# Optimization experiments

Hardware: AMD Instinct MI355X
Metric: run time of the kernel (lower is better)

Reference implementation:

```python
import jax, jax.numpy as jnp
import numpy as np

N_NODES = 100000
N_EDGES = 1600000
NODE_DIM = 3
EDGE_DIM = 32
HIDDEN = 128
OUT_DIM = 3
N_GRAPHS = 64


def _lin(key, fan_in, fan_out):
    k1, k2 = jax.random.split(key)
    s = 1.0 / np.sqrt(fan_in)
    W = jax.random.uniform(k1, (fan_in, fan_out), minval=-s, maxval=s, dtype=jnp.float32)
    b = jax.random.uniform(k2, (fan_out,), minval=-s, maxval=s, dtype=jnp.float32)
    return W, b


def setup_inputs() -> dict:
    key = jax.random.key(0)
    ks = jax.random.split(key, 16)
    x = jax.random.normal(ks[0], (N_NODES, NODE_DIM), dtype=jnp.float32)
    edge_index = jax.random.randint(ks[1], (2, N_EDGES), 0, N_NODES, dtype=jnp.int32)
    edge_attr = jax.random.normal(ks[2], (N_EDGES, EDGE_DIM), dtype=jnp.float32)
    batch = jnp.sort(jax.random.randint(ks[3], (N_NODES,), 0, N_GRAPHS, dtype=jnp.int32))
    # conv1: CGConv at channels=NODE_DIM, in = 2*NODE_DIM + EDGE_DIM
    Wf1, bf1 = _lin(ks[4], 2 * NODE_DIM + EDGE_DIM, NODE_DIM)
    Ws1, bs1 = _lin(ks[5], 2 * NODE_DIM + EDGE_DIM, NODE_DIM)
    Wp, bp = _lin(ks[6], NODE_DIM, HIDDEN)
    # two hidden CGConvs at channels=HIDDEN
    Wf2, bf2 = _lin(ks[7], 2 * HIDDEN + EDGE_DIM, HIDDEN)
    Ws2, bs2 = _lin(ks[8], 2 * HIDDEN + EDGE_DIM, HIDDEN)
    Wf3, bf3 = _lin(ks[9], 2 * HIDDEN + EDGE_DIM, HIDDEN)
    Ws3, bs3 = _lin(ks[10], 2 * HIDDEN + EDGE_DIM, HIDDEN)
    W1, b1 = _lin(ks[11], HIDDEN, HIDDEN)
    W2, b2 = _lin(ks[12], HIDDEN, OUT_DIM)
    return dict(x=x, edge_index=edge_index, edge_attr=edge_attr, batch=batch,
                Wf1=Wf1, bf1=bf1, Ws1=Ws1, bs1=bs1, Wp=Wp, bp=bp,
                Wf2=Wf2, bf2=bf2, Ws2=Ws2, bs2=bs2,
                Wf3=Wf3, bf3=bf3, Ws3=Ws3, bs3=bs3,
                W1=W1, b1=b1, W2=W2, b2=b2)


def _cgconv(x, src, dst, edge_attr, Wf, bf, Ws, bs):
    # z = [x_i (target), x_j (source), e_ij]; message = sigmoid(lin_f(z)) * softplus(lin_s(z))
    z = jnp.concatenate([x[dst], x[src], edge_attr], axis=-1)  # [E, 2C+F]
    m = jax.nn.sigmoid(z @ Wf + bf) * jax.nn.softplus(z @ Ws + bs)  # [E, C]
    agg = jax.ops.segment_sum(m, dst, num_segments=x.shape[0])
    return x + agg


def reference(x, edge_index, edge_attr, batch,
              Wf1, bf1, Ws1, bs1, Wp, bp,
              Wf2, bf2, Ws2, bs2, Wf3, bf3, Ws3, bs3,
              W1, b1, W2, b2):
    src, dst = edge_index[0], edge_index[1]
    h = _cgconv(x, src, dst, edge_attr, Wf1, bf1, Ws1, bs1)
    h = jax.nn.relu(h @ Wp + bp)
    h = jax.nn.relu(_cgconv(h, src, dst, edge_attr, Wf2, bf2, Ws2, bs2))
    h = jax.nn.relu(_cgconv(h, src, dst, edge_attr, Wf3, bf3, Ws3, bs3))
    # global mean pool over graphs
    sums = jax.ops.segment_sum(h, batch, num_segments=N_GRAPHS)
    counts = jax.ops.segment_sum(jnp.ones((h.shape[0],), h.dtype), batch, num_segments=N_GRAPHS)
    pooled = sums / jnp.maximum(counts, 1.0)[:, None]
    g = jax.nn.relu(pooled @ W1 + b1)
    return g @ W2 + b2
```

## Files before the change

kernel.cpp:

```cpp
#include <hip/hip_runtime.h>
#include <hip/hip_bf16.h>


#define N_NODES 100000
#define N_EDGES 1600000
#define HID 128
#define SCAN_BLOCKS 391

typedef unsigned int uint;
typedef short bf16x8 __attribute__((ext_vector_type(8)));
typedef float f32x4 __attribute__((ext_vector_type(4)));

__device__ inline float bflo(uint u) { return __uint_as_float(u << 16); }
__device__ inline float bfhi(uint u) { return __uint_as_float(u & 0xffff0000u); }
__device__ inline uint pack_bf16_2(float a, float b) {
  uint ua = __float_as_uint(a), ub = __float_as_uint(b);
  ua = (ua + 0x7fffu + ((ua >> 16) & 1u)) >> 16;
  ub = (ub + 0x7fffu + ((ub >> 16) & 1u)) >> 16;
  return ua | (ub << 16);
}
__device__ inline float sigmoidf_(float x) {
  return __builtin_amdgcn_rcpf(1.f + __expf(-x));
}
__device__ inline float softplusf_(float x) {
  return fmaxf(x, 0.f) + __logf(1.f + __expf(-fabsf(x)));
}

__global__ __launch_bounds__(256) void hist_k(const int* __restrict__ ei,
                                              int* __restrict__ deg) {
  int e = blockIdx.x * 256 + threadIdx.x;
  if (e >= N_EDGES) return;
  atomicAdd(&deg[ei[N_EDGES + e]], 1);
}

__global__ __launch_bounds__(256) void scan1_k(const int* __restrict__ deg,
                                               int* __restrict__ rowptr,
                                               int* __restrict__ bsums) {
  __shared__ int s[256];
  int i = blockIdx.x * 256 + threadIdx.x;
  int v = (i < N_NODES) ? deg[i] : 0;
  s[threadIdx.x] = v;
  __syncthreads();
  for (int off = 1; off < 256; off <<= 1) {
    int t = (threadIdx.x >= off) ? s[threadIdx.x - off] : 0;
    __syncthreads();
    s[threadIdx.x] += t;
    __syncthreads();
  }
  if (i < N_NODES) rowptr[i] = s[threadIdx.x] - v;
  if (threadIdx.x == 255) bsums[blockIdx.x] = s[255];
}

__global__ __launch_bounds__(512) void scan2_k(int* __restrict__ bsums) {
  __shared__ int s[512];
  int t = threadIdx.x;
  int v = (t < SCAN_BLOCKS) ? bsums[t] : 0;
  s[t] = v;
  __syncthreads();
  for (int off = 1; off < 512; off <<= 1) {
    int x = (t >= off) ? s[t - off] : 0;
    __syncthreads();
    s[t] += x;
    __syncthreads();
  }
  if (t < SCAN_BLOCKS) bsums[t] = s[t] - v;
}

__global__ __launch_bounds__(256) void scan3_k(int* __restrict__ rowptr,
                                               const int* __restrict__ bsums,
                                               int* __restrict__ cur) {
  int i = blockIdx.x * 256 + threadIdx.x;
  if (i < N_NODES) {
    int r = rowptr[i] + bsums[blockIdx.x];
    rowptr[i] = r;
    cur[i] = r;
  }
  if (i == 0) rowptr[N_NODES] = N_EDGES;
}

__global__ __launch_bounds__(256) void scatter_k(const int* __restrict__ ei,
                                                 int* __restrict__ cur,
                                                 uint4* __restrict__ csr) {
  int e = blockIdx.x * 256 + threadIdx.x;
  if (e >= N_EDGES) return;
  int d = ei[N_EDGES + e];
  int pos = atomicAdd(&cur[d], 1);
  csr[pos] = make_uint4((uint)ei[e], (uint)e, (uint)d, 0u);
}

__global__ __launch_bounds__(256) void ea_pack(const float* __restrict__ ea,
                                               const uint4* __restrict__ csr,
                                               uint4* __restrict__ eab) {
  long long t = (long long)blockIdx.x * 256 + threadIdx.x;
  int p = (int)(t >> 2), q = (int)(t & 3);
  if (p >= N_EDGES) return;
  uint e = csr[p].y;
  const float4* er = (const float4*)(ea + (long long)e * 32 + q * 8);
  float4 a0 = er[0], a1 = er[1];
  uint4 pk;
  pk.x = pack_bf16_2(a0.x, a0.y);
  pk.y = pack_bf16_2(a0.z, a0.w);
  pk.z = pack_bf16_2(a1.x, a1.y);
  pk.w = pack_bf16_2(a1.z, a1.w);
  eab[(long long)p * 4 + q] = pk;
}

__global__ __launch_bounds__(256) void conv1_edge(
    const float* __restrict__ x, const int* __restrict__ ei,
    const float* __restrict__ ea,
    const float* __restrict__ Wf, const float* __restrict__ bf,
    const float* __restrict__ Ws, const float* __restrict__ bs,
    float* __restrict__ agg1) {
  int e = blockIdx.x * 256 + threadIdx.x;
  if (e >= N_EDGES) return;
  int src = ei[e], dst = ei[N_EDGES + e];
  float z[38];
#pragma unroll
  for (int k = 0; k < 3; ++k) z[k] = x[dst * 3 + k];
#pragma unroll
  for (int k = 0; k < 3; ++k) z[3 + k] = x[src * 3 + k];
  const float4* er4 = (const float4*)(ea + (long long)e * 32);
#pragma unroll
  for (int k = 0; k < 8; ++k) {
    float4 v = er4[k];
    z[6 + 4 * k + 0] = v.x;
    z[6 + 4 * k + 1] = v.y;
    z[6 + 4 * k + 2] = v.z;
    z[6 + 4 * k + 3] = v.w;
  }
#pragma unroll
  for (int c = 0; c < 3; ++c) {
    float f = bf[c], s = bs[c];
#pragma unroll
    for (int k = 0; k < 38; ++k) {
      f = fmaf(z[k], Wf[k * 3 + c], f);
      s = fmaf(z[k], Ws[k * 3 + c], s);
    }
    atomicAdd(&agg1[dst * 3 + c], sigmoidf_(f) * softplusf_(s));
  }
}

__global__ __launch_bounds__(256) void proj_kernel(
    const float* __restrict__ x, const float* __restrict__ agg1,
    const float* __restrict__ Wp, const float* __restrict__ bp,
    float* __restrict__ h) {
  long long i = (long long)blockIdx.x * 256 + threadIdx.x;
  if (i >= (long long)N_NODES * HID) return;
  int n = (int)(i >> 7), j = (int)(i & 127);
  float v0 = x[n * 3 + 0] + agg1[n * 3 + 0];
  float v1 = x[n * 3 + 1] + agg1[n * 3 + 1];
  float v2 = x[n * 3 + 2] + agg1[n * 3 + 2];
  float acc = bp[j];
  acc = fmaf(v0, Wp[0 * HID + j], acc);
  acc = fmaf(v1, Wp[1 * HID + j], acc);
  acc = fmaf(v2, Wp[2 * HID + j], acc);
  h[i] = fmaxf(acc, 0.f);
}

#define BM 64
#define BK 32

__global__ __launch_bounds__(256) void node_gemm2(
    const float* __restrict__ h, const float* __restrict__ Wf,
    const float* __restrict__ Ws, const float* __restrict__ bf,
    const float* __restrict__ bs, uint* __restrict__ Pb) {
  __shared__ float As[BK][BM + 4];
  __shared__ float BfS[BK][BM + 4];
  __shared__ float BsS[BK][BM + 4];
  int jblk = blockIdx.x;
  int part = jblk >> 1;
  int colbase = (jblk & 1) * 64;
  int rowoff = part * 128;
  int m0 = blockIdx.y * BM;
  int tid = threadIdx.x, tx = tid & 15, ty = tid >> 4;
  float accF[4][4] = {}, accS[4][4] = {};
  for (int k0 = 0; k0 < 128; k0 += BK) {
#pragma unroll
    for (int i = 0; i < 2; ++i) {
      int f = tid + i * 256;
      int r = f >> 3, c4 = (f & 7) * 4;
      float4 v = {0.f, 0.f, 0.f, 0.f};
      int row = m0 + r;
      if (row < N_NODES)
        v = *(const float4*)&h[(long long)row * 128 + k0 + c4];
      As[c4 + 0][r] = v.x; As[c4 + 1][r] = v.y;
      As[c4 + 2][r] = v.z; As[c4 + 3][r] = v.w;
    }
#pragma unroll
    for (int i = 0; i < 2; ++i) {
      int f = tid + i * 256;
      int r = f >> 4, c4 = (f & 15) * 4;
      *(float4*)&BfS[r][c4] =
          *(const float4*)&Wf[(long long)(k0 + r + rowoff) * 128 + colbase + c4];
      *(float4*)&BsS[r][c4] =
          *(const float4*)&Ws[(long long)(k0 + r + rowoff) * 128 + colbase + c4];
    }
    __syncthreads();
#pragma unroll
    for (int k = 0; k < BK; ++k) {
      float4 a = *(const float4*)&As[k][ty * 4];
      float4 bF = *(const float4*)&BfS[k][tx * 4];
      float4 bS = *(const float4*)&BsS[k][tx * 4];
      float av[4] = {a.x, a.y, a.z, a.w};
      float bFv[4] = {bF.x, bF.y, bF.z, bF.w};
      float bSv[4] = {bS.x, bS.y, bS.z, bS.w};
#pragma unroll
      for (int i = 0; i < 4; ++i)
#pragma unroll
        for (int j = 0; j < 4; ++j) {
          accF[i][j] = fmaf(av[i], bFv[j], accF[i][j]);
          accS[i][j] = fmaf(av[i], bSv[j], accS[i][j]);
        }
    }
    __syncthreads();
  }
  float fbias[4] = {0.f, 0.f, 0.f, 0.f}, sbias[4] = {0.f, 0.f, 0.f, 0.f};
  if (part == 0) {
#pragma unroll
    for (int j = 0; j < 4; ++j) {
      fbias[j] = bf[colbase + tx * 4 + j];
      sbias[j] = bs[colbase + tx * 4 + j];
    }
  }
#pragma unroll
  for (int i = 0; i < 4; ++i) {
    int row = m0 + ty * 4 + i;
    if (row < N_NODES) {
      uint4 o;
      o.x = pack_bf16_2(accF[i][0] + fbias[0], accS[i][0] + sbias[0]);
      o.y = pack_bf16_2(accF[i][1] + fbias[1], accS[i][1] + sbias[1]);
      o.z = pack_bf16_2(accF[i][2] + fbias[2], accS[i][2] + sbias[2]);
      o.w = pack_bf16_2(accF[i][3] + fbias[3], accS[i][3] + sbias[3]);
      *(uint4*)&Pb[(long long)row * 256 + part * 128 + colbase + tx * 4] = o;
    }
  }
}

__global__ __launch_bounds__(256) void w_prep(const float* __restrict__ Wf,
                                              const float* __restrict__ Ws,
                                              uint* __restrict__ Btg) {
  int t = threadIdx.x;
  const float* W = (t < 128) ? Wf : Ws;
  int c = t & 127;
#pragma unroll
  for (int kk = 0; kk < 16; ++kk) {
    float a = W[(256 + 2 * kk) * 128 + c];
    float b = W[(256 + 2 * kk + 1) * 128 + c];
    Btg[t * 16 + kk] = pack_bf16_2(a, b);
  }
}

#define EMSG_EB 64
#define LSTR 20
#define CAP 16
__global__ __launch_bounds__(256, 4) void edge_msg(
    const uint* __restrict__ Pb, const uint4* __restrict__ eab,
    const uint* __restrict__ Btg, const uint4* __restrict__ csr,
    const int* __restrict__ rowptr, float* __restrict__ h) {
  __shared__ uint Alds[EMSG_EB * LSTR];
  __shared__ uint Blds[256 * LSTR];
  __shared__ float accL[CAP * 128];
  __shared__ int dstL[64], srcL[64], liL[64];
  __shared__ int dlist[CAP], compL[CAP];
  __shared__ int nDistS;
  int tid = threadIdx.x;
  int j0 = blockIdx.x * EMSG_EB;
  {
    int r = tid >> 2, q = tid & 3;
    uint4 v = eab[(long long)j0 * 4 + tid];
    *(uint4*)&Alds[r * LSTR + q * 4] = v;
  }
  {
    const uint4* s4 = (const uint4*)(Btg + tid * 16);
    uint4 v0 = s4[0], v1 = s4[1], v2 = s4[2], v3 = s4[3];
    uint* d = &Blds[tid * LSTR];
    *(uint4*)(d + 0) = v0; *(uint4*)(d + 4) = v1;
    *(uint4*)(d + 8) = v2; *(uint4*)(d + 12) = v3;
  }
#pragma unroll
  for (int i = 0; i < (CAP * 128) / 256; ++i) accL[tid + i * 256] = 0.f;
  if (tid < 64) {
    uint4 cj = csr[j0 + tid];
    int d = (int)cj.z;
    dstL[tid] = d;
    srcL[tid] = (int)cj.x;
    int dprev = __shfl_up(d, 1, 64);
    bool flag = (tid == 0) || (d != dprev);
    unsigned long long m = __ballot(flag);
    unsigned long long pre = (tid == 63) ? ~0ull : ((1ull << (tid + 1)) - 1);
    int li = __popcll(m & pre) - 1;
    liL[tid] = li;
    if (flag && li < CAP) {
      dlist[li] = d;
      int r0 = rowptr[d], r1 = rowptr[d + 1];
      compL[li] = ((r0 == j0 + tid) && (r1 <= j0 + EMSG_EB)) ? 1 : 0;
    }
    if (tid == 0) nDistS = __popcll(m);
  }
  __syncthreads();
  int wave = tid >> 6, lane = tid & 63;
  int c0w = wave * 32;
  int l15 = lane & 15, lq = lane >> 4;
  bf16x8 afr[4], bfr[4];
#pragma unroll
  for (int mt = 0; mt < 4; ++mt)
    afr[mt] = *(const bf16x8*)&Alds[(mt * 16 + l15) * LSTR + lq * 4];
  int chs0 = c0w + l15, chs1 = c0w + 16 + l15;
  bfr[0] = *(const bf16x8*)&Blds[chs0 * LSTR + lq * 4];
  bfr[1] = *(const bf16x8*)&Blds[chs1 * LSTR + lq * 4];
  bfr[2] = *(const bf16x8*)&Blds[(128 + chs0) * LSTR + lq * 4];
  bfr[3] = *(const bf16x8*)&Blds[(128 + chs1) * LSTR + lq * 4];
  f32x4 acc[4][4];
#pragma unroll
  for (int mt = 0; mt < 4; ++mt)
#pragma unroll
    for (int nt = 0; nt < 4; ++nt) {
      f32x4 z = {0.f, 0.f, 0.f, 0.f};
      acc[mt][nt] = __builtin_amdgcn_mfma_f32_16x16x32_bf16(afr[mt], bfr[nt], z, 0, 0, 0);
    }
#pragma unroll
  for (int mt = 0; mt < 4; ++mt) {
    int o = mt * 16 + lq * 4;
    int dsts[4], lis[4];
#pragma unroll
    for (int reg = 0; reg < 4; ++reg) {
      dsts[reg] = dstL[o + reg];
      lis[reg] = liL[o + reg];
    }
#pragma unroll
    for (int cp = 0; cp < 2; ++cp) {
      int c = (cp ? chs1 : chs0);
      float mr[4];
#pragma unroll
      for (int reg = 0; reg < 4; ++reg) {
        uint gd = Pb[(long long)dsts[reg] * 256 + c];
        uint gs = Pb[(long long)srcL[o + reg] * 256 + 128 + c];
        float f = acc[mt][cp][reg] + bflo(gd) + bflo(gs);
        float s = acc[mt][2 + cp][reg] + bfhi(gd) + bfhi(gs);
        mr[reg] = sigmoidf_(f) * softplusf_(s);
      }
      float racc = mr[0];
      int cl = lis[0], cd = dsts[0];
#pragma unroll
      for (int reg = 1; reg < 4; ++reg) {
        if (lis[reg] == cl) {
          racc += mr[reg];
        } else {
          if (cl < CAP) atomicAdd(&accL[cl * 128 + c], racc);
          else atomicAdd(&h[(long long)cd * HID + c], racc);
          cl = lis[reg]; cd = dsts[reg]; racc = mr[reg];
        }
      }
      if (cl < CAP) atomicAdd(&accL[cl * 128 + c], racc);
      else atomicAdd(&h[(long long)cd * HID + c], racc);
    }
  }
  __syncthreads();
  int nD = nDistS;
  if (nD > CAP) nD = CAP;
  int c = tid & 127;
  for (int li = tid >> 7; li < nD; li += 2) {
    int d = dlist[li];
    float v = accL[li * 128 + c];
    float* hp = &h[(long long)d * HID + c];
    if (compL[li]) {
      *hp = fmaxf(*hp + v, 0.f);
    } else {
      atomicAdd(hp, v);
    }
  }
}

__global__ __launch_bounds__(256) void relu_k(float* __restrict__ h) {
  const int total = N_NODES * HID / 4;
  for (int i = blockIdx.x * 256 + threadIdx.x; i < total; i += gridDim.x * 256) {
    float4 v = ((float4*)h)[i];
    v.x = fmaxf(v.x, 0.f); v.y = fmaxf(v.y, 0.f);
    v.z = fmaxf(v.z, 0.f); v.w = fmaxf(v.w, 0.f);
    ((float4*)h)[i] = v;
  }
}

#define POOL_NODES 128
__global__ __launch_bounds__(128) void pool2(
    const float* __restrict__ h, const int* __restrict__ batch,
    float* __restrict__ sums, float* __restrict__ cnts) {
  int n0 = blockIdx.x * POOL_NODES;
  if (n0 >= N_NODES) return;
  int t = threadIdx.x;
  int nEnd = n0 + POOL_NODES;
  if (nEnd > N_NODES) nEnd = N_NODES;
  float acc = 0.f;
  int bcur = batch[n0];
  int cnt = 0;
  for (int n = n0; n < nEnd; ++n) {
    int b = batch[n];
    if (b != bcur) {
      atomicAdd(&sums[bcur * HID + t], acc);
      if (t == 0) atomicAdd(&cnts[bcur], (float)cnt);
      acc = 0.f; cnt = 0; bcur = b;
    }
    acc += h[(long long)n * HID + t];
    ++cnt;
  }
  atomicAdd(&sums[bcur * HID + t], acc);
  if (t == 0) atomicAdd(&cnts[bcur], (float)cnt);
}

__global__ __launch_bounds__(128) void mlpA(
    const float* __restrict__ sums, const float* __restrict__ cnts,
    const float* __restrict__ W1, const float* __restrict__ b1,
    float* __restrict__ g) {
  __shared__ float pl[HID];
  int gr = blockIdx.x, j = threadIdx.x;
  float cnt = fmaxf(cnts[gr], 1.f);
  pl[j] = sums[gr * HID + j] / cnt;
  __syncthreads();
  float acc = b1[j];
#pragma unroll 8
  for (int k = 0; k < HID; ++k) acc = fmaf(pl[k], W1[k * HID + j], acc);
  g[gr * HID + j] = fmaxf(acc, 0.f);
}

__global__ __launch_bounds__(256) void mlpB(
    const float* __restrict__ g, const float* __restrict__ W2,
    const float* __restrict__ b2, float* __restrict__ out) {
  int t = threadIdx.x;
  if (t >= 64 * 3) return;
  int gr = t / 3, o = t % 3;
  float acc = b2[o];
#pragma unroll 8
  for (int k = 0; k < HID; ++k) acc = fmaf(g[gr * HID + k], W2[k * 3 + o], acc);
  out[t] = acc;
}

extern "C" void kernel_launch(void* const* d_in, const int* in_sizes, int n_in,
                              void* d_out, int out_size, void* d_ws, size_t ws_size,
                              hipStream_t stream) {
  const float* x   = (const float*)d_in[0];
  const int*   ei  = (const int*)d_in[1];
  const float* ea  = (const float*)d_in[2];
  const int*   bat = (const int*)d_in[3];
  const float* Wf1 = (const float*)d_in[4];
  const float* bf1 = (const float*)d_in[5];
  const float* Ws1 = (const float*)d_in[6];
  const float* bs1 = (const float*)d_in[7];
  const float* Wp  = (const float*)d_in[8];
  const float* bp  = (const float*)d_in[9];
  const float* Wf2 = (const float*)d_in[10];
  const float* bf2 = (const float*)d_in[11];
  const float* Ws2 = (const float*)d_in[12];
  const float* bs2 = (const float*)d_in[13];
  const float* Wf3 = (const float*)d_in[14];
  const float* bf3 = (const float*)d_in[15];
  const float* Ws3 = (const float*)d_in[16];
  const float* bs3 = (const float*)d_in[17];
  const float* W1  = (const float*)d_in[18];
  const float* b1  = (const float*)d_in[19];
  const float* W2  = (const float*)d_in[20];
  const float* b2  = (const float*)d_in[21];
  float* out = (float*)d_out;

  char* w = (char*)d_ws;
  size_t off = 0;
  auto alloc = [&](size_t bytes) {
    void* p = w + off;
    off += (bytes + 255) & ~(size_t)255;
    return p;
  };
  int*   deg    = (int*)alloc((size_t)N_NODES * 4);
  int*   rowptr = (int*)alloc((size_t)(N_NODES + 1) * 4);
  int*   cur    = (int*)alloc((size_t)N_NODES * 4);
  int*   bsums  = (int*)alloc((size_t)512 * 4);
  uint4* csr    = (uint4*)alloc((size_t)N_EDGES * 16);
  float* agg1   = (float*)alloc((size_t)N_NODES * 3 * 4);
  float* h      = (float*)alloc((size_t)N_NODES * HID * 4);
  uint*  Pb     = (uint*)alloc((size_t)N_NODES * 256 * 4);
  uint4* eab    = (uint4*)alloc((size_t)N_EDGES * 64);
  float* sums   = (float*)alloc((size_t)64 * HID * 4);
  float* cnts   = (float*)alloc((size_t)64 * 4);
  float* g      = (float*)alloc((size_t)64 * HID * 4);
  uint*  Btg    = (uint*)alloc((size_t)256 * 16 * 4);
  (void)ws_size;

  hipMemsetAsync(deg, 0, (size_t)N_NODES * 4, stream);
  hist_k<<<(N_EDGES + 255) / 256, 256, 0, stream>>>(ei, deg);
  scan1_k<<<SCAN_BLOCKS, 256, 0, stream>>>(deg, rowptr, bsums);
  scan2_k<<<1, 512, 0, stream>>>(bsums);
  scan3_k<<<SCAN_BLOCKS, 256, 0, stream>>>(rowptr, bsums, cur);
  scatter_k<<<(N_EDGES + 255) / 256, 256, 0, stream>>>(ei, cur, csr);
  ea_pack<<<(N_EDGES * 4 + 255) / 256, 256, 0, stream>>>(ea, csr, eab);

  hipMemsetAsync(agg1, 0, (size_t)N_NODES * 3 * 4, stream);
  conv1_edge<<<(N_EDGES + 255) / 256, 256, 0, stream>>>(x, ei, ea, Wf1, bf1, Ws1, bs1, agg1);
  proj_kernel<<<(N_NODES * HID + 255) / 256, 256, 0, stream>>>(x, agg1, Wp, bp, h);

  dim3 ngrid2(4, (N_NODES + BM - 1) / BM);
  int eblocks = N_EDGES / EMSG_EB;

  node_gemm2<<<ngrid2, 256, 0, stream>>>(h, Wf2, Ws2, bf2, bs2, Pb);
  w_prep<<<1, 256, 0, stream>>>(Wf2, Ws2, Btg);
  edge_msg<<<eblocks, 256, 0, stream>>>(Pb, eab, Btg, csr, rowptr, h);
  relu_k<<<4096, 256, 0, stream>>>(h);

  node_gemm2<<<ngrid2, 256, 0, stream>>>(h, Wf3, Ws3, bf3, bs3, Pb);
  w_prep<<<1, 256, 0, stream>>>(Wf3, Ws3, Btg);
  edge_msg<<<eblocks, 256, 0, stream>>>(Pb, eab, Btg, csr, rowptr, h);
  relu_k<<<4096, 256, 0, stream>>>(h);

  hipMemsetAsync(sums, 0, (size_t)(64 * HID + 64) * 4, stream);
  pool2<<<(N_NODES + POOL_NODES - 1) / POOL_NODES, POOL_NODES, 0, stream>>>(h, bat, sums, cnts);
  mlpA<<<64, 128, 0, stream>>>(sums, cnts, W1, b1, g);
  mlpB<<<1, 256, 0, stream>>>(g, W2, b2, out);
}
```

Measured before the change: 2.038 ms.

## Switch node GEMM to bf16 MFMA with bf16 activation copy; simplify edge atomics

Replaces the fp32 SIMT node GEMM with an MFMA bf16 kernel that reads a packed bf16 copy of h, produced by the projection and ReLU kernels, plus pre-packed weights. This removes the fp32 FMA-bound GEMM and halves its input bandwidth. In exchange it adds the bf16 copy writes and a weight-prep launch, and lowers GEMM input precision. The edge message kernel also drops its run-length merging of same-destination values and issues one atomic per edge value.

```diff
diff --git a/kernel.cpp b/kernel.cpp
--- a/kernel.cpp
+++ b/kernel.cpp
@@ -140,98 +140,105 @@
   }
 }
 
-__global__ __launch_bounds__(256) void proj_kernel(
+__global__ __launch_bounds__(256) void proj2(
     const float* __restrict__ x, const float* __restrict__ agg1,
     const float* __restrict__ Wp, const float* __restrict__ bp,
-    float* __restrict__ h) {
+    float* __restrict__ h, uint* __restrict__ hb) {
   long long i = (long long)blockIdx.x * 256 + threadIdx.x;
-  if (i >= (long long)N_NODES * HID) return;
-  int n = (int)(i >> 7), j = (int)(i & 127);
+  if (i >= (long long)N_NODES * 64) return;
+  int n = (int)(i >> 6), jp = (int)(i & 63);
+  int j0 = jp * 2;
   float v0 = x[n * 3 + 0] + agg1[n * 3 + 0];
   float v1 = x[n * 3 + 1] + agg1[n * 3 + 1];
   float v2 = x[n * 3 + 2] + agg1[n * 3 + 2];
-  float acc = bp[j];
-  acc = fmaf(v0, Wp[0 * HID + j], acc);
-  acc = fmaf(v1, Wp[1 * HID + j], acc);
-  acc = fmaf(v2, Wp[2 * HID + j], acc);
-  h[i] = fmaxf(acc, 0.f);
-}
-
-#define BM 64
-#define BK 32
-
-__global__ __launch_bounds__(256) void node_gemm2(
-    const float* __restrict__ h, const float* __restrict__ Wf,
-    const float* __restrict__ Ws, const float* __restrict__ bf,
-    const float* __restrict__ bs, uint* __restrict__ Pb) {
-  __shared__ float As[BK][BM + 4];
-  __shared__ float BfS[BK][BM + 4];
-  __shared__ float BsS[BK][BM + 4];
-  int jblk = blockIdx.x;
-  int part = jblk >> 1;
-  int colbase = (jblk & 1) * 64;
-  int rowoff = part * 128;
-  int m0 = blockIdx.y * BM;
-  int tid = threadIdx.x, tx = tid & 15, ty = tid >> 4;
-  float accF[4][4] = {}, accS[4][4] = {};
-  for (int k0 = 0; k0 < 128; k0 += BK) {
-#pragma unroll
-    for (int i = 0; i < 2; ++i) {
-      int f = tid + i * 256;
-      int r = f >> 3, c4 = (f & 7) * 4;
-      float4 v = {0.f, 0.f, 0.f, 0.f};
-      int row = m0 + r;
-      if (row < N_NODES)
-        v = *(const float4*)&h[(long long)row * 128 + k0 + c4];
-      As[c4 + 0][r] = v.x; As[c4 + 1][r] = v.y;
-      As[c4 + 2][r] = v.z; As[c4 + 3][r] = v.w;
-    }
-#pragma unroll
-    for (int i = 0; i < 2; ++i) {
-      int f = tid + i * 256;
-      int r = f >> 4, c4 = (f & 15) * 4;
-      *(float4*)&BfS[r][c4] =
-          *(const float4*)&Wf[(long long)(k0 + r + rowoff) * 128 + colbase + c4];
-      *(float4*)&BsS[r][c4] =
-          *(const float4*)&Ws[(long long)(k0 + r + rowoff) * 128 + colbase + c4];
-    }
-    __syncthreads();
-#pragma unroll
-    for (int k = 0; k < BK; ++k) {
-      float4 a = *(const float4*)&As[k][ty * 4];
-      float4 bF = *(const float4*)&BfS[k][tx * 4];
-      float4 bS = *(const float4*)&BsS[k][tx * 4];
-      float av[4] = {a.x, a.y, a.z, a.w};
-      float bFv[4] = {bF.x, bF.y, bF.z, bF.w};
-      float bSv[4] = {bS.x, bS.y, bS.z, bS.w};
-#pragma unroll
-      for (int i = 0; i < 4; ++i)
-#pragma unroll
-        for (int j = 0; j < 4; ++j) {
-          accF[i][j] = fmaf(av[i], bFv[j], accF[i][j]);
-          accS[i][j] = fmaf(av[i], bSv[j], accS[i][j]);
-        }
-    }
-    __syncthreads();
-  }
-  float fbias[4] = {0.f, 0.f, 0.f, 0.f}, sbias[4] = {0.f, 0.f, 0.f, 0.f};
-  if (part == 0) {
-#pragma unroll
-    for (int j = 0; j < 4; ++j) {
-      fbias[j] = bf[colbase + tx * 4 + j];
-      sbias[j] = bs[colbase + tx * 4 + j];
-    }
-  }
-#pragma unroll
-  for (int i = 0; i < 4; ++i) {
-    int row = m0 + ty * 4 + i;
+  float a0 = bp[j0], a1 = bp[j0 + 1];
+  a0 = fmaf(v0, Wp[0 * HID + j0], a0);
+  a0 = fmaf(v1, Wp[1 * HID + j0], a0);
+  a0 = fmaf(v2, Wp[2 * HID + j0], a0);
+  a1 = fmaf(v0, Wp[0 * HID + j0 + 1], a1);
+  a1 = fmaf(v1, Wp[1 * HID + j0 + 1], a1);
+  a1 = fmaf(v2, Wp[2 * HID + j0 + 1], a1);
+  a0 = fmaxf(a0, 0.f);
+  a1 = fmaxf(a1, 0.f);
+  *(float2*)&h[(long long)n * HID + j0] = make_float2(a0, a1);
+  hb[(long long)n * 64 + jp] = pack_bf16_2(a0, a1);
+}
+
+__global__ __launch_bounds__(256) void w_prep2(const float* __restrict__ Wf,
+                                               const float* __restrict__ Ws,
+                                               uint* __restrict__ Wpk) {
+  int row = blockIdx.x * 256 + threadIdx.x;
+  int pm = row >> 7;
+  int c = row & 127;
+  const float* W = (pm & 1) ? Ws : Wf;
+  int rowoff = (pm >> 1) * 128;
+  for (int kk = 0; kk < 64; ++kk) {
+    float a = W[(rowoff + 2 * kk) * 128 + c];
+    float b = W[(rowoff + 2 * kk + 1) * 128 + c];
+    Wpk[row * 64 + kk] = pack_bf16_2(a, b);
+  }
+}
+
+#define NG_STR 68
+__global__ __launch_bounds__(256, 4) void node_gemmM(
+    const uint* __restrict__ hb, const uint* __restrict__ Wpk,
+    const float* __restrict__ bf, const float* __restrict__ bs,
+    uint* __restrict__ Pb) {
+  __shared__ uint Alds[64 * NG_STR];
+  int part = blockIdx.x;
+  int m0 = blockIdx.y * 64;
+  int tid = threadIdx.x;
+  {
+    int r = tid >> 2, q = tid & 3;
+    int row = m0 + r;
+    uint* d = &Alds[r * NG_STR + q * 16];
     if (row < N_NODES) {
-      uint4 o;
-      o.x = pack_bf16_2(accF[i][0] + fbias[0], accS[i][0] + sbias[0]);
-      o.y = pack_bf16_2(accF[i][1] + fbias[1], accS[i][1] + sbias[1]);
-      o.z = pack_bf16_2(accF[i][2] + fbias[2], accS[i][2] + sbias[2]);
-      o.w = pack_bf16_2(accF[i][3] + fbias[3], accS[i][3] + sbias[3]);
-      *(uint4*)&Pb[(long long)row * 256 + part * 128 + colbase + tx * 4] = o;
+      const uint4* s4 = (const uint4*)&hb[(long long)row * 64 + q * 16];
+      uint4 v0 = s4[0], v1 = s4[1], v2 = s4[2], v3 = s4[3];
+      *(uint4*)(d + 0) = v0; *(uint4*)(d + 4) = v1;
+      *(uint4*)(d + 8) = v2; *(uint4*)(d + 12) = v3;
+    } else {
+      uint4 z = make_uint4(0, 0, 0, 0);
+      *(uint4*)(d + 0) = z; *(uint4*)(d + 4) = z;
+      *(uint4*)(d + 8) = z; *(uint4*)(d + 12) = z;
+    }
+  }
+  __syncthreads();
+  int wave = tid >> 6, lane = tid & 63;
+  int l15 = lane & 15, lq = lane >> 4;
+  int arow = wave * 16 + l15;
+  const uint* WpF = Wpk + (part * 2 + 0) * 128 * 64;
+  const uint* WpS = Wpk + (part * 2 + 1) * 128 * 64;
+  f32x4 accF[8], accS[8];
+#pragma unroll
+  for (int nt = 0; nt < 8; ++nt) {
+    f32x4 z = {0.f, 0.f, 0.f, 0.f};
+    accF[nt] = z;
+    accS[nt] = z;
+  }
+#pragma unroll
+  for (int ks = 0; ks < 4; ++ks) {
+    bf16x8 afr = *(const bf16x8*)&Alds[arow * NG_STR + ks * 16 + lq * 4];
+#pragma unroll
+    for (int nt = 0; nt < 8; ++nt) {
+      bf16x8 bF = *(const bf16x8*)&WpF[(nt * 16 + l15) * 64 + ks * 16 + lq * 4];
+      bf16x8 bS = *(const bf16x8*)&WpS[(nt * 16 + l15) * 64 + ks * 16 + lq * 4];
+      accF[nt] = __builtin_amdgcn_mfma_f32_16x16x32_bf16(afr, bF, accF[nt], 0, 0, 0);
+      accS[nt] = __builtin_amdgcn_mfma_f32_16x16x32_bf16(afr, bS, accS[nt], 0, 0, 0);
+    }
+  }
+#pragma unroll
+  for (int nt = 0; nt < 8; ++nt) {
+    int c = nt * 16 + l15;
+    float fb = (part == 0) ? bf[c] : 0.f;
+    float sb = (part == 0) ? bs[c] : 0.f;
+#pragma unroll
+    for (int reg = 0; reg < 4; ++reg) {
+      int node = m0 + wave * 16 + lq * 4 + reg;
+      if (node < N_NODES) {
+        Pb[(long long)node * 256 + part * 128 + c] =
+            pack_bf16_2(accF[nt][reg] + fb, accS[nt][reg] + sb);
+      }
     }
   }
 }
@@ -321,38 +328,29 @@
 #pragma unroll
   for (int mt = 0; mt < 4; ++mt) {
     int o = mt * 16 + lq * 4;
-    int dsts[4], lis[4];
+    int dsts[4], srcs[4], lis[4];
 #pragma unroll
     for (int reg = 0; reg < 4; ++reg) {
       dsts[reg] = dstL[o + reg];
+      srcs[reg] = srcL[o + reg];
       lis[reg] = liL[o + reg];
     }
 #pragma unroll
     for (int cp = 0; cp < 2; ++cp) {
       int c = (cp ? chs1 : chs0);
-      float mr[4];
 #pragma unroll
       for (int reg = 0; reg < 4; ++reg) {
         uint gd = Pb[(long long)dsts[reg] * 256 + c];
-        uint gs = Pb[(long long)srcL[o + reg] * 256 + 128 + c];
+        uint gs = Pb[(long long)srcs[reg] * 256 + 128 + c];
         float f = acc[mt][cp][reg] + bflo(gd) + bflo(gs);
         float s = acc[mt][2 + cp][reg] + bfhi(gd) + bfhi(gs);
-        mr[reg] = sigmoidf_(f) * softplusf_(s);
-      }
-      float racc = mr[0];
-      int cl = lis[0], cd = dsts[0];
-#pragma unroll
-      for (int reg = 1; reg < 4; ++reg) {
-        if (lis[reg] == cl) {
-          racc += mr[reg];
+        float mr = sigmoidf_(f) * softplusf_(s);
+        if (lis[reg] < CAP) {
+          atomicAdd(&accL[lis[reg] * 128 + c], mr);
         } else {
-          if (cl < CAP) atomicAdd(&accL[cl * 128 + c], racc);
-          else atomicAdd(&h[(long long)cd * HID + c], racc);
-          cl = lis[reg]; cd = dsts[reg]; racc = mr[reg];
+          atomicAdd(&h[(long long)dsts[reg] * HID + c], mr);
         }
       }
-      if (cl < CAP) atomicAdd(&accL[cl * 128 + c], racc);
-      else atomicAdd(&h[(long long)cd * HID + c], racc);
     }
   }
   __syncthreads();
@@ -368,6 +366,21 @@
     } else {
       atomicAdd(hp, v);
     }
+  }
+}
+
+__global__ __launch_bounds__(256) void relu2(float* __restrict__ h,
+                                             uint* __restrict__ hb) {
+  const int total = N_NODES * 32;
+  for (int i = blockIdx.x * 256 + threadIdx.x; i < total; i += gridDim.x * 256) {
+    float4 v = ((float4*)h)[i];
+    v.x = fmaxf(v.x, 0.f); v.y = fmaxf(v.y, 0.f);
+    v.z = fmaxf(v.z, 0.f); v.w = fmaxf(v.w, 0.f);
+    ((float4*)h)[i] = v;
+    uint2 o;
+    o.x = pack_bf16_2(v.x, v.y);
+    o.y = pack_bf16_2(v.z, v.w);
+    *(uint2*)&hb[(long long)i * 2] = o;
   }
 }
 
@@ -475,12 +488,14 @@
   uint4* csr    = (uint4*)alloc((size_t)N_EDGES * 16);
   float* agg1   = (float*)alloc((size_t)N_NODES * 3 * 4);
   float* h      = (float*)alloc((size_t)N_NODES * HID * 4);
+  uint*  hb     = (uint*)alloc((size_t)N_NODES * 64 * 4);
   uint*  Pb     = (uint*)alloc((size_t)N_NODES * 256 * 4);
   uint4* eab    = (uint4*)alloc((size_t)N_EDGES * 64);
   float* sums   = (float*)alloc((size_t)64 * HID * 4);
   float* cnts   = (float*)alloc((size_t)64 * 4);
   float* g      = (float*)alloc((size_t)64 * HID * 4);
   uint*  Btg    = (uint*)alloc((size_t)256 * 16 * 4);
+  uint*  Wpk    = (uint*)alloc((size_t)512 * 64 * 4);
   (void)ws_size;
 
   hipMemsetAsync(deg, 0, (size_t)N_NODES * 4, stream);
@@ -493,17 +508,19 @@
 
   hipMemsetAsync(agg1, 0, (size_t)N_NODES * 3 * 4, stream);
   conv1_edge<<<(N_EDGES + 255) / 256, 256, 0, stream>>>(x, ei, ea, Wf1, bf1, Ws1, bs1, agg1);
-  proj_kernel<<<(N_NODES * HID + 255) / 256, 256, 0, stream>>>(x, agg1, Wp, bp, h);
-
-  dim3 ngrid2(4, (N_NODES + BM - 1) / BM);
+  proj2<<<(N_NODES * 64 + 255) / 256, 256, 0, stream>>>(x, agg1, Wp, bp, h, hb);
+
+  dim3 nggrid(2, (N_NODES + 63) / 64);
   int eblocks = N_EDGES / EMSG_EB;
 
-  node_gemm2<<<ngrid2, 256, 0, stream>>>(h, Wf2, Ws2, bf2, bs2, Pb);
+  w_prep2<<<2, 256, 0, stream>>>(Wf2, Ws2, Wpk);
+  node_gemmM<<<nggrid, 256, 0, stream>>>(hb, Wpk, bf2, bs2, Pb);
   w_prep<<<1, 256, 0, stream>>>(Wf2, Ws2, Btg);
   edge_msg<<<eblocks, 256, 0, stream>>>(Pb, eab, Btg, csr, rowptr, h);
-  relu_k<<<4096, 256, 0, stream>>>(h);
-
-  node_gemm2<<<ngrid2, 256, 0, stream>>>(h, Wf3, Ws3, bf3, bs3, Pb);
+  relu2<<<4096, 256, 0, stream>>>(h, hb);
+
+  w_prep2<<<2, 256, 0, stream>>>(Wf3, Ws3, Wpk);
+  node_gemmM<<<nggrid, 256, 0, stream>>>(hb, Wpk, bf3, bs3, Pb);
   w_prep<<<1, 256, 0, stream>>>(Wf3, Ws3, Btg);
   edge_msg<<<eblocks, 256, 0, stream>>>(Pb, eab, Btg, csr, rowptr, h);
   relu_k<<<4096, 256, 0, stream>>>(h);
```

New measurement: 3.340 ms. 63.8% more time.
